# Optimization experiments

Measured on AMD Instinct MI355X. Metric: run time of the kernel, lower is better.

## Reference

```python
import jax, jax.numpy as jnp
import numpy as np

N = 50000       # num nodes
E = 600000      # num edges
IN = 128        # in_channels
H = 4           # heads
C = 32          # out_channels per head
B = 3           # num bends (Bezier control points)
NEG_SLOPE = 0.2


def setup_inputs() -> dict:
    key = jax.random.key(0)
    ks = jax.random.split(key, 6)
    x = jax.random.normal(ks[0], (N, IN), dtype=jnp.float32)
    edge_index = jax.random.randint(ks[1], (2, E), 0, N)
    # Bezier coefficients at t=0.5 for a 3-point curve: [0.25, 0.5, 0.25]
    coeffs_t = jnp.array([0.25, 0.5, 0.25], dtype=jnp.float32)
    glorot_w = float(np.sqrt(2.0) * np.sqrt(6.0 / (H * C + IN)))
    glorot_a = float(np.sqrt(2.0) * np.sqrt(6.0 / (1 + C)))
    lin_weight = jax.random.uniform(ks[2], (B, H * C, IN), jnp.float32, -glorot_w, glorot_w)
    lin_bias = jnp.zeros((B, H * C), dtype=jnp.float32)
    att_src = jax.random.uniform(ks[3], (B, 1, H, C), jnp.float32, -glorot_a, glorot_a)
    att_dst = jax.random.uniform(ks[4], (B, 1, H, C), jnp.float32, -glorot_a, glorot_a)
    return {"x": x, "edge_index": edge_index, "coeffs_t": coeffs_t,
            "lin_weight": lin_weight, "lin_bias": lin_bias,
            "att_src": att_src, "att_dst": att_dst}


def reference(x, edge_index, coeffs_t, lin_weight, lin_bias, att_src, att_dst):
    # Bezier parameter interpolation: weighted sum over bends
    W = jnp.einsum('b,boi->oi', coeffs_t, lin_weight)      # [H*C, IN]
    bias = jnp.einsum('b,bo->o', coeffs_t, lin_bias)       # [H*C]
    a_src = jnp.einsum('b,bqhc->qhc', coeffs_t, att_src)   # [1,H,C]
    a_dst = jnp.einsum('b,bqhc->qhc', coeffs_t, att_dst)   # [1,H,C]

    n = x.shape[0]
    xt = (x @ W.T + bias).reshape(n, H, C)                 # [N,H,C]
    alpha_src = jnp.sum(xt * a_src, axis=-1)               # [N,H]
    alpha_dst = jnp.sum(xt * a_dst, axis=-1)               # [N,H]

    row, col = edge_index[0], edge_index[1]
    alpha = alpha_src[row] + alpha_dst[col]                # [E,H]
    alpha = jax.nn.leaky_relu(alpha, NEG_SLOPE)

    # scatter-softmax over incoming edges of each target node (col)
    amax = jax.ops.segment_max(alpha, col, num_segments=n)  # [N,H]
    ex = jnp.exp(alpha - amax[col])                         # [E,H]
    denom = jax.ops.segment_sum(ex, col, num_segments=n)    # [N,H]
    alpha = ex / (denom[col] + 1e-16)                       # [E,H]

    # weighted neighbor aggregation (edge-parallel segment reduction)
    msg = xt[row] * alpha[..., None]                        # [E,H,C]
    out = jax.ops.segment_sum(msg, col, num_segments=n)     # [N,H,C]
    return out.reshape(n, H * C)                            # concat=True
```

## Files before the change

kernel.cpp:

```cpp
#include <hip/hip_runtime.h>
#include <hip/hip_bf16.h>

#define GAT_IN   128
#define GAT_OUT  128
#define GAT_H    4
#define GAT_C    32
#define NEG_SLOPE 0.2f
#define BUCKET   48

typedef __attribute__((ext_vector_type(8))) short bf16x8;
typedef __attribute__((ext_vector_type(4))) float f32x4;
union U4 { uint4 u; bf16x8 v; };

static __device__ __forceinline__ unsigned int pack_bf16(float lo, float hi) {
    __hip_bfloat16 a = __float2bfloat16(lo);
    __hip_bfloat16 b = __float2bfloat16(hi);
    unsigned short ua = *reinterpret_cast<unsigned short*>(&a);
    unsigned short ub = *reinterpret_cast<unsigned short*>(&b);
    return (unsigned int)ua | ((unsigned int)ub << 16);
}

__global__ __launch_bounds__(256) void bucket_interp_kernel(
    const int* __restrict__ ei, int* __restrict__ cnt,
    int* __restrict__ esrc, int ne,
    const float* __restrict__ coeffs,
    const float* __restrict__ lw,
    const float* __restrict__ lb,
    const float* __restrict__ asr,
    const float* __restrict__ ads,
    unsigned int* __restrict__ wfrag,
    float* __restrict__ biasc,
    float* __restrict__ asrc, float* __restrict__ adst)
{
    int b = blockIdx.x;
    if (b < 32) {
        int i = b * 256 + threadIdx.x;
        float c0 = coeffs[0], c1 = coeffs[1], c2 = coeffs[2];
        int lane = (i >> 2) & 63;
        int nk   = i >> 8;
        int jw   = i & 3;
        int nt = nk >> 2, ks = nk & 3;
        int o = nt * 16 + (lane & 15);
        int k = ks * 32 + (lane >> 4) * 8 + jw * 2;
        int idx = o * 128 + k;
        float w0 = c0 * lw[idx]     + c1 * lw[16384 + idx]     + c2 * lw[32768 + idx];
        float w1 = c0 * lw[idx + 1] + c1 * lw[16384 + idx + 1] + c2 * lw[32768 + idx + 1];
        wfrag[i] = pack_bf16(w0, w1);
        if (b == 0 && threadIdx.x < 128) {
            int t = threadIdx.x;
            biasc[t] = c0 * lb[t]  + c1 * lb[128 + t]  + c2 * lb[256 + t];
            asrc[t]  = c0 * asr[t] + c1 * asr[128 + t] + c2 * asr[256 + t];
            adst[t]  = c0 * ads[t] + c1 * ads[128 + t] + c2 * ads[256 + t];
        }
        return;
    }
    int e = (b - 32) * 256 + threadIdx.x;
    if (e >= ne) return;
    int row = ei[e], col = ei[ne + e];
    int pos = atomicAdd(&cnt[col], 1);
    if (pos < BUCKET) esrc[col * BUCKET + pos] = row;
}

__global__ __launch_bounds__(256) void gemm_alpha_kernel(
    const float* __restrict__ x,
    const unsigned int* __restrict__ wfrag,
    const float* __restrict__ biasc,
    const float* __restrict__ asrc,
    const float* __restrict__ adst,
    unsigned int* __restrict__ xtb,
    float* __restrict__ alpha_src,
    float* __restrict__ alpha_dst,
    int n)
{
    __shared__ __align__(16) float C[64 * 132];
    int tid  = threadIdx.x;
    int lane = tid & 63;
    int wave = tid >> 6;
    int quad = lane >> 4;
    int lm   = lane & 15;
    int m0   = blockIdx.x * 64 + wave * 16;

    f32x4 acc[8];
    #pragma unroll
    for (int t = 0; t < 8; ++t) acc[t] = (f32x4){0.f, 0.f, 0.f, 0.f};

    int arow = m0 + lm; if (arow >= n) arow = n - 1;
    const float4* xr = (const float4*)(x + (size_t)arow * 128 + quad * 8);
    const uint4*  wf = (const uint4*)wfrag;

    #pragma unroll
    for (int ks = 0; ks < 4; ++ks) {
        float4 a0 = xr[ks * 8 + 0];
        float4 a1 = xr[ks * 8 + 1];
        U4 af;
        af.u.x = pack_bf16(a0.x, a0.y);
        af.u.y = pack_bf16(a0.z, a0.w);
        af.u.z = pack_bf16(a1.x, a1.y);
        af.u.w = pack_bf16(a1.z, a1.w);
        #pragma unroll
        for (int nt = 0; nt < 8; ++nt) {
            U4 bf; bf.u = wf[(nt * 4 + ks) * 64 + lane];
            acc[nt] = __builtin_amdgcn_mfma_f32_16x16x32_bf16(
                af.v, bf.v, acc[nt], 0, 0, 0);
        }
    }

    #pragma unroll
    for (int nt = 0; nt < 8; ++nt) {
        int col = nt * 16 + lm;
        #pragma unroll
        for (int r = 0; r < 4; ++r) {
            int rowl = wave * 16 + quad * 4 + r;
            C[rowl * 132 + col] = acc[nt][r];
        }
    }
    __syncthreads();

    int rowl = wave * 16 + (lane >> 2);
    int seg  = lane & 3;
    int mrow = blockIdx.x * 64 + rowl;
    if (mrow < n) {
        const float4* cb = (const float4*)(C + rowl * 132 + seg * 32);
        const float4* bb = (const float4*)(biasc + seg * 32);
        const float4* sb = (const float4*)(asrc + seg * 32);
        const float4* db = (const float4*)(adst + seg * 32);
        float s = 0.f, d = 0.f;
        unsigned int ow[16];
        #pragma unroll
        for (int q = 0; q < 8; ++q) {
            float4 v = cb[q];
            float4 b = bb[q];
            v.x += b.x; v.y += b.y; v.z += b.z; v.w += b.w;
            float4 as = sb[q], ad = db[q];
            s += v.x * as.x + v.y * as.y + v.z * as.z + v.w * as.w;
            d += v.x * ad.x + v.y * ad.y + v.z * ad.z + v.w * ad.w;
            ow[q * 2 + 0] = pack_bf16(v.x, v.y);
            ow[q * 2 + 1] = pack_bf16(v.z, v.w);
        }
        alpha_src[mrow * 4 + seg] = s;
        alpha_dst[mrow * 4 + seg] = d;
        uint4* xo = (uint4*)(xtb + (size_t)mrow * 64 + seg * 16);
        #pragma unroll
        for (int q4 = 0; q4 < 4; ++q4)
            xo[q4] = make_uint4(ow[q4 * 4], ow[q4 * 4 + 1],
                                ow[q4 * 4 + 2], ow[q4 * 4 + 3]);
    }
}

static __device__ __forceinline__ void window16(
    int4 ra, int4 rb, int4 rc, int4 rd, int rem,
    unsigned int h, unsigned int sl, float ad,
    const unsigned int* __restrict__ xtb,
    const float* __restrict__ alpha_src,
    float& den, float4& acc)
{
    int r[16];
    r[0]=ra.x;  r[1]=ra.y;  r[2]=ra.z;  r[3]=ra.w;
    r[4]=rb.x;  r[5]=rb.y;  r[6]=rb.z;  r[7]=rb.w;
    r[8]=rc.x;  r[9]=rc.y;  r[10]=rc.z; r[11]=rc.w;
    r[12]=rd.x; r[13]=rd.y; r[14]=rd.z; r[15]=rd.w;
    #pragma unroll
    for (int t = 0; t < 16; ++t) r[t] = (t < rem) ? r[t] : 0;

    float as[16];
    #pragma unroll
    for (int t = 0; t < 16; ++t)
        as[t] = alpha_src[(((unsigned)r[t]) << 2) | h];
    uint2 u[16];
    #pragma unroll
    for (int t = 0; t < 16; ++t)
        u[t] = *(const uint2*)(xtb + ((((unsigned)r[t]) << 6) + (sl << 1)));

    float e[16];
    #pragma unroll
    for (int t = 0; t < 16; ++t) {
        float a = as[t] + ad;
        a = fmaxf(a, NEG_SLOPE * a);
        float ex = __expf(a);
        e[t] = (t < rem) ? ex : 0.f;
    }
    float s01 = e[0]+e[1],   s23 = e[2]+e[3],   s45 = e[4]+e[5],   s67 = e[6]+e[7];
    float s89 = e[8]+e[9],   sab = e[10]+e[11], scd = e[12]+e[13], sef = e[14]+e[15];
    den += ((s01+s23) + (s45+s67)) + ((s89+sab) + (scd+sef));

    #pragma unroll
    for (int t = 0; t < 16; ++t) {
        acc.x = fmaf(e[t], __uint_as_float(u[t].x << 16),          acc.x);
        acc.y = fmaf(e[t], __uint_as_float(u[t].x & 0xFFFF0000u),  acc.y);
        acc.z = fmaf(e[t], __uint_as_float(u[t].y << 16),          acc.z);
        acc.w = fmaf(e[t], __uint_as_float(u[t].y & 0xFFFF0000u),  acc.w);
    }
}

__global__ __launch_bounds__(256) void agg_kernel(
    const int* __restrict__ cnt,
    const int* __restrict__ esrc,
    const unsigned int* __restrict__ xtb,
    const float* __restrict__ alpha_src,
    const float* __restrict__ alpha_dst,
    float* __restrict__ out,
    int n)
{
    int wave = threadIdx.x >> 6;
    unsigned int lane = threadIdx.x & 63;
    unsigned int sub = lane >> 5;
    unsigned int sl  = lane & 31;
    int node = blockIdx.x * 8 + wave * 2 + (int)sub;
    bool active = node < n;
    int nodec = active ? node : 0;
    unsigned int h = sl >> 3;

    const int4* ebq = (const int4*)(esrc + nodec * BUCKET);
    int4 ra = ebq[0];
    int4 rb = ebq[1];
    int4 rc = ebq[2];
    int4 rd = ebq[3];
    int   m  = cnt[nodec];
    float ad = alpha_dst[((unsigned)nodec << 2) | h];
    if (!active) m = 0;
    if (m > BUCKET) m = BUCKET;

    float4 acc = make_float4(0.f, 0.f, 0.f, 0.f);
    float den = 0.f;

    window16(ra, rb, rc, rd, m, h, sl, ad, xtb, alpha_src, den, acc);

    for (int j = 16; j < m; j += 16) {
        int q = j >> 2;
        int4 wa = ebq[q], wb = ebq[q + 1], wc = ebq[q + 2], wd = ebq[q + 3];
        window16(wa, wb, wc, wd, m - j, h, sl, ad, xtb, alpha_src, den, acc);
    }

    if (active) {
        float inv = 1.0f / (den + 1e-16f);
        ((float4*)out)[((unsigned)node << 5) | sl] =
            make_float4(acc.x * inv, acc.y * inv, acc.z * inv, acc.w * inv);
    }
}

extern "C" void kernel_launch(void* const* d_in, const int* in_sizes, int n_in,
                              void* d_out, int out_size, void* d_ws, size_t ws_size,
                              hipStream_t stream)
{
    const float* x      = (const float*)d_in[0];
    const int*   ei     = (const int*)  d_in[1];
    const float* coeffs = (const float*)d_in[2];
    const float* lw     = (const float*)d_in[3];
    const float* lb     = (const float*)d_in[4];
    const float* asr    = (const float*)d_in[5];
    const float* ads    = (const float*)d_in[6];
    float* out = (float*)d_out;

    int n  = in_sizes[0] / GAT_IN;
    int ne = in_sizes[1] / 2;

    float* ws        = (float*)d_ws;
    unsigned int* wfrag = (unsigned int*)ws;
    float* biasc     = ws + 16384;
    float* asrc      = ws + 16512;
    float* adst      = ws + 16640;
    unsigned int* xtb = (unsigned int*)(ws + 16768);
    float* alpha_src = (float*)(xtb + (size_t)n * 64);
    float* alpha_dst = alpha_src + (size_t)n * 4;
    int*   cnt       = (int*)(alpha_dst + (size_t)n * 4);
    int*   esrc      = cnt + n;

    hipMemsetAsync(cnt, 0, (size_t)n * sizeof(int), stream);
    bucket_interp_kernel<<<32 + (ne + 255) / 256, 256, 0, stream>>>(
        ei, cnt, esrc, ne, coeffs, lw, lb, asr, ads, wfrag, biasc, asrc, adst);
    gemm_alpha_kernel<<<(n + 63) / 64, 256, 0, stream>>>(
        x, wfrag, biasc, asrc, adst, xtb, alpha_src, alpha_dst, n);
    agg_kernel<<<(n + 7) / 8, 256, 0, stream>>>(
        cnt, esrc, xtb, alpha_src, alpha_dst, out, n);
}
```

Measured before the change: 167.2 us.

## Fuse GEMM, bucketing and aggregation into one cooperative persistent kernel

Replaces the memset, bucket and GEMM launch sequence with a small interp+zero kernel followed by one cooperative persistent kernel. That kernel interleaves the GEMM and edge-bucketing work units, does a grid-wide sync, then runs the aggregation. The aim is to cut launch overhead and let bucketing overlap with the GEMM. In exchange, occupancy is capped by cooperative residency and the grid barrier adds a cost. Shared memory for the GEMM tile also limits how many blocks fit per CU.

```diff
diff --git a/kernel.cpp b/kernel.cpp
--- a/kernel.cpp
+++ b/kernel.cpp
@@ -1,5 +1,8 @@
 #include <hip/hip_runtime.h>
 #include <hip/hip_bf16.h>
+#include <hip/hip_cooperative_groups.h>
+
+namespace cg = cooperative_groups;
 
 #define GAT_IN   128
 #define GAT_OUT  128
@@ -20,9 +23,7 @@
     return (unsigned int)ua | ((unsigned int)ub << 16);
 }
 
-__global__ __launch_bounds__(256) void bucket_interp_kernel(
-    const int* __restrict__ ei, int* __restrict__ cnt,
-    int* __restrict__ esrc, int ne,
+__global__ __launch_bounds__(256) void interp_zero_kernel(
     const float* __restrict__ coeffs,
     const float* __restrict__ lw,
     const float* __restrict__ lb,
@@ -30,11 +31,12 @@
     const float* __restrict__ ads,
     unsigned int* __restrict__ wfrag,
     float* __restrict__ biasc,
-    float* __restrict__ asrc, float* __restrict__ adst)
-{
-    int b = blockIdx.x;
+    float* __restrict__ asrc, float* __restrict__ adst,
+    int* __restrict__ cnt, int n)
+{
+    int b = blockIdx.x, t = threadIdx.x;
     if (b < 32) {
-        int i = b * 256 + threadIdx.x;
+        int i = b * 256 + t;
         float c0 = coeffs[0], c1 = coeffs[1], c2 = coeffs[2];
         int lane = (i >> 2) & 63;
         int nk   = i >> 8;
@@ -46,22 +48,18 @@
         float w0 = c0 * lw[idx]     + c1 * lw[16384 + idx]     + c2 * lw[32768 + idx];
         float w1 = c0 * lw[idx + 1] + c1 * lw[16384 + idx + 1] + c2 * lw[32768 + idx + 1];
         wfrag[i] = pack_bf16(w0, w1);
-        if (b == 0 && threadIdx.x < 128) {
-            int t = threadIdx.x;
+        if (b == 0 && t < 128) {
             biasc[t] = c0 * lb[t]  + c1 * lb[128 + t]  + c2 * lb[256 + t];
             asrc[t]  = c0 * asr[t] + c1 * asr[128 + t] + c2 * asr[256 + t];
             adst[t]  = c0 * ads[t] + c1 * ads[128 + t] + c2 * ads[256 + t];
         }
-        return;
-    }
-    int e = (b - 32) * 256 + threadIdx.x;
-    if (e >= ne) return;
-    int row = ei[e], col = ei[ne + e];
-    int pos = atomicAdd(&cnt[col], 1);
-    if (pos < BUCKET) esrc[col * BUCKET + pos] = row;
-}
-
-__global__ __launch_bounds__(256) void gemm_alpha_kernel(
+    }
+    for (int idx = b * 256 + t; idx < n; idx += gridDim.x * 256)
+        cnt[idx] = 0;
+}
+
+static __device__ __forceinline__ void gemm_body(
+    int bu, float* C,
     const float* __restrict__ x,
     const unsigned int* __restrict__ wfrag,
     const float* __restrict__ biasc,
@@ -72,13 +70,12 @@
     float* __restrict__ alpha_dst,
     int n)
 {
-    __shared__ __align__(16) float C[64 * 132];
     int tid  = threadIdx.x;
     int lane = tid & 63;
     int wave = tid >> 6;
     int quad = lane >> 4;
     int lm   = lane & 15;
-    int m0   = blockIdx.x * 64 + wave * 16;
+    int m0   = bu * 64 + wave * 16;
 
     f32x4 acc[8];
     #pragma unroll
@@ -118,7 +115,7 @@
 
     int rowl = wave * 16 + (lane >> 2);
     int seg  = lane & 3;
-    int mrow = blockIdx.x * 64 + rowl;
+    int mrow = bu * 64 + rowl;
     if (mrow < n) {
         const float4* cb = (const float4*)(C + rowl * 132 + seg * 32);
         const float4* bb = (const float4*)(biasc + seg * 32);
@@ -145,6 +142,19 @@
             xo[q4] = make_uint4(ow[q4 * 4], ow[q4 * 4 + 1],
                                 ow[q4 * 4 + 2], ow[q4 * 4 + 3]);
     }
+    __syncthreads();
+}
+
+static __device__ __forceinline__ void bucket_body(
+    int bu, const int* __restrict__ ei,
+    int* __restrict__ cnt, int* __restrict__ esrc, int ne)
+{
+    int e = bu * 256 + threadIdx.x;
+    if (e < ne) {
+        int row = ei[e], col = ei[ne + e];
+        int pos = atomicAdd(&cnt[col], 1);
+        if (pos < BUCKET) esrc[col * BUCKET + pos] = row;
+    }
 }
 
 static __device__ __forceinline__ void window16(
@@ -192,7 +202,8 @@
     }
 }
 
-__global__ __launch_bounds__(256) void agg_kernel(
+static __device__ __forceinline__ void agg_body(
+    int bu,
     const int* __restrict__ cnt,
     const int* __restrict__ esrc,
     const unsigned int* __restrict__ xtb,
@@ -205,7 +216,7 @@
     unsigned int lane = threadIdx.x & 63;
     unsigned int sub = lane >> 5;
     unsigned int sl  = lane & 31;
-    int node = blockIdx.x * 8 + wave * 2 + (int)sub;
+    int node = bu * 8 + wave * 2 + (int)sub;
     bool active = node < n;
     int nodec = active ? node : 0;
     unsigned int h = sl >> 3;
@@ -236,6 +247,43 @@
         ((float4*)out)[((unsigned)node << 5) | sl] =
             make_float4(acc.x * inv, acc.y * inv, acc.z * inv, acc.w * inv);
     }
+}
+
+__global__ __launch_bounds__(256) void fused_kernel(
+    const float* __restrict__ x,
+    const unsigned int* __restrict__ wfrag,
+    const float* __restrict__ biasc,
+    const float* __restrict__ asrc,
+    const float* __restrict__ adst,
+    unsigned int* __restrict__ xtb,
+    float* __restrict__ alpha_src,
+    float* __restrict__ alpha_dst,
+    const int* __restrict__ ei,
+    int* __restrict__ cnt,
+    int* __restrict__ esrc,
+    float* __restrict__ out,
+    int n, int ne)
+{
+    __shared__ __align__(16) float C[64 * 132];
+    int G = gridDim.x;
+    int gemm_units   = (n + 63) >> 6;
+    int bucket_units = (ne + 255) >> 8;
+
+    for (int u = blockIdx.x; u < gemm_units + bucket_units; u += G) {
+        if (u < gemm_units)
+            gemm_body(u, C, x, wfrag, biasc, asrc, adst,
+                      xtb, alpha_src, alpha_dst, n);
+        else
+            bucket_body(u - gemm_units, ei, cnt, esrc, ne);
+    }
+
+    __threadfence();
+    cg::this_grid().sync();
+    __threadfence();
+
+    int agg_units = (n + 7) >> 3;
+    for (int u = blockIdx.x; u < agg_units; u += G)
+        agg_body(u, cnt, esrc, xtb, alpha_src, alpha_dst, out, n);
 }
 
 extern "C" void kernel_launch(void* const* d_in, const int* in_sizes, int n_in,
@@ -265,11 +313,29 @@
     int*   cnt       = (int*)(alpha_dst + (size_t)n * 4);
     int*   esrc      = cnt + n;
 
-    hipMemsetAsync(cnt, 0, (size_t)n * sizeof(int), stream);
-    bucket_interp_kernel<<<32 + (ne + 255) / 256, 256, 0, stream>>>(
-        ei, cnt, esrc, ne, coeffs, lw, lb, asr, ads, wfrag, biasc, asrc, adst);
-    gemm_alpha_kernel<<<(n + 63) / 64, 256, 0, stream>>>(
-        x, wfrag, biasc, asrc, adst, xtb, alpha_src, alpha_dst, n);
-    agg_kernel<<<(n + 7) / 8, 256, 0, stream>>>(
-        cnt, esrc, xtb, alpha_src, alpha_dst, out, n);
-}
+    interp_zero_kernel<<<256, 256, 0, stream>>>(
+        coeffs, lw, lb, asr, ads, wfrag, biasc, asrc, adst, cnt, n);
+
+    static int gridB = 0;
+    if (gridB == 0) {
+        int blocksPerCU = 0;
+        if (hipOccupancyMaxActiveBlocksPerMultiprocessor(
+                &blocksPerCU, reinterpret_cast<const void*>(&fused_kernel),
+                256, 0) != hipSuccess || blocksPerCU < 1)
+            blocksPerCU = 2;
+        int cus = 0;
+        if (hipDeviceGetAttribute(&cus, hipDeviceAttributeMultiprocessorCount,
+                                  0) != hipSuccess || cus < 1)
+            cus = 256;
+        gridB = blocksPerCU * cus;
+        if (gridB > 6250) gridB = 6250;
+    }
+    void* kargs[] = {
+        (void*)&x, (void*)&wfrag, (void*)&biasc, (void*)&asrc, (void*)&adst,
+        (void*)&xtb, (void*)&alpha_src, (void*)&alpha_dst,
+        (void*)&ei, (void*)&cnt, (void*)&esrc, (void*)&out,
+        (void*)&n, (void*)&ne
+    };
+    hipLaunchCooperativeKernel(reinterpret_cast<const void*>(&fused_kernel),
+                               dim3(gridB), dim3(256), kargs, 0, stream);
+}
```

After: 285.0 us. 70.5% more time.
